# Kernel tuning notes

Hardware: AMD Instinct MI355X
Metric: run time of the kernel (lower is better)

The kernel has to match this reference:

```python
import jax, jax.numpy as jnp
import numpy as np

SPLINE_ORDER = 3
GRID_SIZE = 16
IN_DIM = 64
OUT_DIM = 64
BATCH = 1024
GRID_RANGE = (-1.0, 1.0)


def make_grid():
    low, up = GRID_RANGE
    spacing = (up - low) / GRID_SIZE
    g = jnp.arange(-SPLINE_ORDER, GRID_SIZE + SPLINE_ORDER + 1, dtype=jnp.float32)
    g = g * spacing + low  # (grid_size + 2k + 1,)
    return jnp.broadcast_to(g[None, None, :], (OUT_DIM, IN_DIM, g.shape[0]))


def setup_inputs() -> dict:
    key = jax.random.key(0)
    kx, kc = jax.random.split(key)
    x = jax.random.uniform(kx, (BATCH, IN_DIM), dtype=jnp.float32)
    coef = jax.random.normal(kc, (OUT_DIM, IN_DIM, GRID_SIZE + SPLINE_ORDER), dtype=jnp.float32)
    grid = make_grid()
    return {"x": x, "coef": coef, "grid": grid}


def bspline_bases(x, grid, k):
    # x: (B, in_dim) -> broadcast against grid (out, in, G+2k+1)
    xg = x[:, None, :, None]          # (B, 1, in, 1)
    g = grid[None, ...]               # (1, out, in, G+2k+1)
    bases = ((xg >= g[..., :-1]) & (xg < g[..., 1:])).astype(x.dtype)  # order-0
    for j in range(1, k + 1):
        left = (xg - g[..., :-(j + 1)]) / (g[..., j:-1] - g[..., :-(j + 1)]) * bases[..., :-1]
        right = (g[..., j + 1:] - xg) / (g[..., j + 1:] - g[..., 1:-j]) * bases[..., 1:]
        bases = left + right
    return bases  # (B, out, in, G+k)


def reference(x, coef, grid):
    bases = bspline_bases(x, grid, SPLINE_ORDER)        # (B, out, in, G+k)
    spline = jnp.sum(bases * coef[None, ...], axis=-1)  # (B, out, in)
    return spline
```

## Files before the change

### kernel.cpp

```cpp
#include <hip/hip_runtime.h>


#define BATCH   1024
#define IN_DIM  64
#define OUT_DIM 64
#define NCOEF   19

__global__ __launch_bounds__(256) void kan_kernel(
    const float* __restrict__ x,
    const float* __restrict__ coef,
    float* __restrict__ out)
{
    __shared__ float sw[IN_DIM][4];
    __shared__ int   scb[IN_DIM];

    const int b   = blockIdx.x;
    const int tid = threadIdx.x;

    if (tid < IN_DIM) {
        float xv = x[b * IN_DIM + tid];
        float xf = xv * 8.0f;
        int   t0 = (int)floorf(xf);
        t0 = max(0, min(7, t0));
        float u  = xf - (float)t0;
        float v  = 1.0f - u;
        float u2 = u * u, u3 = u2 * u;
        const float k6 = 1.0f / 6.0f;
        sw[tid][0] = v * v * v * k6;
        sw[tid][1] = (3.0f*u3 - 6.0f*u2 + 4.0f) * k6;
        sw[tid][2] = (-3.0f*u3 + 3.0f*u2 + 3.0f*u + 1.0f) * k6;
        sw[tid][3] = u3 * k6;
        scb[tid]   = tid * NCOEF + t0 + 8;
    }
    __syncthreads();

    const int i  = tid & 63;
    const int o0 = tid >> 6;

    const float w0 = sw[i][0], w1 = sw[i][1], w2 = sw[i][2], w3 = sw[i][3];
    const int   cb = scb[i];

    const float* cp = coef + cb;
    float*       op = out + (size_t)b * (OUT_DIM * IN_DIM) + i;

    #pragma unroll
    for (int o = o0; o < OUT_DIM; o += 4) {
        const float* c = cp + o * (IN_DIM * NCOEF);
        float s = w0 * c[0];
        s = fmaf(w1, c[1], s);
        s = fmaf(w2, c[2], s);
        s = fmaf(w3, c[3], s);
        op[o * IN_DIM] = s;
    }
}

extern "C" void kernel_launch(void* const* d_in, const int* in_sizes, int n_in,
                              void* d_out, int out_size, void* d_ws, size_t ws_size,
                              hipStream_t stream) {
    const float* x    = (const float*)d_in[0];
    const float* coef = (const float*)d_in[1];
    float* out = (float*)d_out;

    dim3 grid(BATCH), block(256);
    kan_kernel<<<grid, block, 0, stream>>>(x, coef, out);
}
```

Measured before the change: 70.42 us.

## Tile batch and output dims, stage coefficient slab in shared memory

The grid is reorganised into 2D tiles of 16 batch rows by 8 output rows. Each block copies its 8×64×19 coefficient slab into LDS once with float4 loads, then reuses it across 16 batch rows instead of re-gathering coefficients from global or L2 for every batch. Output stores become nontemporal to avoid polluting cache with the 16 MB write stream. The cost is about 39 KB of LDS per block, which can limit occupancy, plus a serial per-block preload phase and possible LDS bank conflicts on the data-dependent coefficient gather.

```diff
diff --git a/kernel.cpp b/kernel.cpp
--- a/kernel.cpp
+++ b/kernel.cpp
@@ -5,20 +5,33 @@
 #define IN_DIM  64
 #define OUT_DIM 64
 #define NCOEF   19
+#define BT      16
+#define OT      8
 
 __global__ __launch_bounds__(256) void kan_kernel(
     const float* __restrict__ x,
     const float* __restrict__ coef,
     float* __restrict__ out)
 {
-    __shared__ float sw[IN_DIM][4];
-    __shared__ int   scb[IN_DIM];
+    __shared__ float scoef[OT * IN_DIM * NCOEF];
+    __shared__ float sw[BT][IN_DIM][4];
+    __shared__ int   st0[BT][IN_DIM];
 
-    const int b   = blockIdx.x;
     const int tid = threadIdx.x;
+    const int b0  = blockIdx.x * BT;
+    const int o0  = blockIdx.y * OT;
 
-    if (tid < IN_DIM) {
-        float xv = x[b * IN_DIM + tid];
+    {
+        const float4* csrc = (const float4*)(coef + (size_t)o0 * IN_DIM * NCOEF);
+        float4* cdst = (float4*)scoef;
+        const int n4 = OT * IN_DIM * NCOEF / 4;
+        for (int v = tid; v < n4; v += 256)
+            cdst[v] = csrc[v];
+    }
+
+    for (int p = tid; p < BT * IN_DIM; p += 256) {
+        const int bb = p >> 6, i = p & 63;
+        float xv = x[(b0 + bb) * IN_DIM + i];
         float xf = xv * 8.0f;
         int   t0 = (int)floorf(xf);
         t0 = max(0, min(7, t0));
@@ -26,31 +39,36 @@
         float v  = 1.0f - u;
         float u2 = u * u, u3 = u2 * u;
         const float k6 = 1.0f / 6.0f;
-        sw[tid][0] = v * v * v * k6;
-        sw[tid][1] = (3.0f*u3 - 6.0f*u2 + 4.0f) * k6;
-        sw[tid][2] = (-3.0f*u3 + 3.0f*u2 + 3.0f*u + 1.0f) * k6;
-        sw[tid][3] = u3 * k6;
-        scb[tid]   = tid * NCOEF + t0 + 8;
+        sw[bb][i][0] = v * v * v * k6;
+        sw[bb][i][1] = (3.0f*u3 - 6.0f*u2 + 4.0f) * k6;
+        sw[bb][i][2] = (-3.0f*u3 + 3.0f*u2 + 3.0f*u + 1.0f) * k6;
+        sw[bb][i][3] = u3 * k6;
+        st0[bb][i]   = i * NCOEF + t0 + 8;
     }
     __syncthreads();
 
-    const int i  = tid & 63;
-    const int o0 = tid >> 6;
+    const int i = tid & 63;
+    const int g = tid >> 6;
 
-    const float w0 = sw[i][0], w1 = sw[i][1], w2 = sw[i][2], w3 = sw[i][3];
-    const int   cb = scb[i];
+    float* op = out + (size_t)b0 * (OUT_DIM * IN_DIM) + (size_t)o0 * IN_DIM + i;
 
-    const float* cp = coef + cb;
-    float*       op = out + (size_t)b * (OUT_DIM * IN_DIM) + i;
+    for (int bb = 0; bb < BT; ++bb) {
+        const float w0 = sw[bb][i][0];
+        const float w1 = sw[bb][i][1];
+        const float w2 = sw[bb][i][2];
+        const float w3 = sw[bb][i][3];
+        const int   cb = st0[bb][i];
+        float* obp = op + (size_t)bb * (OUT_DIM * IN_DIM);
 
-    #pragma unroll
-    for (int o = o0; o < OUT_DIM; o += 4) {
-        const float* c = cp + o * (IN_DIM * NCOEF);
-        float s = w0 * c[0];
-        s = fmaf(w1, c[1], s);
-        s = fmaf(w2, c[2], s);
-        s = fmaf(w3, c[3], s);
-        op[o * IN_DIM] = s;
+        #pragma unroll
+        for (int oo = g; oo < OT; oo += 4) {
+            const float* c = scoef + oo * (IN_DIM * NCOEF) + cb;
+            float s = w0 * c[0];
+            s = fmaf(w1, c[1], s);
+            s = fmaf(w2, c[2], s);
+            s = fmaf(w3, c[3], s);
+            __builtin_nontemporal_store(s, obp + oo * IN_DIM);
+        }
     }
 }
 
@@ -61,6 +79,6 @@
     const float* coef = (const float*)d_in[1];
     float* out = (float*)d_out;
 
-    dim3 grid(BATCH), block(256);
+    dim3 grid(BATCH / BT, OUT_DIM / OT), block(256);
     kan_kernel<<<grid, block, 0, stream>>>(x, coef, out);
 }
```

Result: faster. 68.59 us (-2.6%).
